# Kernel tuning notes

Measured on AMD Instinct MI355X. Metric: run time of the kernel, lower is better.

Reference implementation:

```python
import jax, jax.numpy as jnp
import numpy as np

INV_DELTA = 15.0  # inv_delta init kwarg


def setup_inputs() -> dict:
    key = jax.random.key(0)
    k1, k2 = jax.random.split(key)
    features = jax.random.normal(k1, (64, 1024, 14, 14), dtype=jnp.float32)
    # torch init: randn(num_words, num_channels).clamp(min=0)
    embedding = jnp.clip(jax.random.normal(k2, (8192, 1024), dtype=jnp.float32), 0.0, None)
    min_distance_mean = jnp.ones((1,), dtype=jnp.float32) * 0.5  # buffer init
    return {"features": features, "embedding": embedding,
            "min_distance_mean": min_distance_mean}


def reference(features, embedding, min_distance_mean):
    # BoWExtractor.forward in eval mode (no dictionary queue update / EMA).
    f = features[:, :, 1:-1, 1:-1]                      # [B,C,12,12] crop border
    emb_sq = jnp.sum(embedding * embedding, axis=1)     # [K]  ||w_k||^2
    cross = jnp.einsum('bchw,kc->bkhw', f, embedding)   # 1x1 conv == GEMM
    # squared L2 distance to every codeword: [B,K,12,12]
    dist = jnp.sum(f * f, axis=1, keepdims=True) - 2.0 * cross \
           + emb_sq[None, :, None, None]
    inv_delta_adaptive = INV_DELTA / min_distance_mean[0]
    codes = jax.nn.softmax(-inv_delta_adaptive * dist, axis=1)  # soft assignment over K
    bow = jnp.max(codes, axis=(2, 3))                   # global max-pool -> [B,K]
    bow = bow / jnp.sum(jnp.abs(bow), axis=1, keepdims=True)  # L1 normalize
    return bow, codes
```

## Files before the change

kernel.cpp:

```cpp
#include <hip/hip_runtime.h>
#include <math.h>

#define BB   64
#define CC   1024
#define HWC  144
#define KK   8192
#define MM   9216
#define NBN  64

typedef __attribute__((ext_vector_type(8))) short          bf16x8;
typedef __attribute__((ext_vector_type(8))) unsigned short u16x8;
typedef __attribute__((ext_vector_type(4))) float          f32x4;

#define FA_BYTES  ((size_t)MM * CC * 2 * 2)
#define FB_BYTES  ((size_t)KK * CC * 2 * 2)
#define OFF_FA    0
#define OFF_FB    (OFF_FA + FA_BYTES)
#define OFF_ESQ   (OFF_FB + FB_BYTES)
#define OFF_PM    (OFF_ESQ + (size_t)KK * 4)
#define OFF_PS    (OFF_PM + (size_t)NBN * MM * 4)
#define OFF_FACT  (OFF_PS + (size_t)NBN * MM * 4)

__device__ inline unsigned short f2bf(float x) {
    union { float f; unsigned u; } v; v.f = x;
    unsigned r = v.u + 0x7fffu + ((v.u >> 16) & 1u);
    return (unsigned short)(r >> 16);
}
__device__ inline float bf2f(unsigned short h) {
    union { unsigned u; float f; } v; v.u = (unsigned)h << 16;
    return v.f;
}

__global__ __launch_bounds__(256)
void prep_A(const float* __restrict__ feat, u16x8* __restrict__ fA) {
    __shared__ float tile[64][145];
    int cb = blockIdx.x;
    int b  = blockIdx.y;
    for (int idx = threadIdx.x; idx < 64 * 144; idx += 256) {
        int r = idx / 144, hw = idx - r * 144;
        int h = hw / 12, w = hw - h * 12;
        tile[r][hw] = feat[(size_t)((b * 1024 + cb * 64 + r) * 196)
                           + (h + 1) * 14 + (w + 1)];
    }
    __syncthreads();
    for (int idx = threadIdx.x; idx < 8 * 144; idx += 256) {
        int g = idx / 144, hw = idx - g * 144;
        int p = b * 144 + hw;
        int bm = p >> 7, row = p & 127;
        int cg = cb * 64 + g * 8;
        int kt = cg >> 5, chunk = (cg >> 3) & 3;
        u16x8 hi, lo;
#pragma unroll
        for (int e = 0; e < 8; ++e) {
            float x = tile[g * 8 + e][hw];
            unsigned short h16 = f2bf(x);
            hi[e] = (short)h16;
            lo[e] = (short)f2bf(x - bf2f(h16));
        }
        size_t base = ((size_t)(bm * 32 + kt) * 2) * 512 + chunk * 128 + row;
        fA[base] = hi;
        fA[base + 512] = lo;
    }
}

__global__ __launch_bounds__(256)
void prep_B(const float* __restrict__ emb, u16x8* __restrict__ fB) {
    __shared__ float tile[128][65];
    int cb = blockIdx.x;
    int bn = blockIdx.y;
#pragma unroll
    for (int i = 0; i < 8; ++i) {
        int idx = threadIdx.x + i * 256;
        int nl = idx >> 4, c4 = idx & 15;
        const float4 v = *reinterpret_cast<const float4*>(
            emb + (size_t)(bn * 128 + nl) * 1024 + cb * 64 + c4 * 4);
        tile[nl][c4 * 4 + 0] = v.x;
        tile[nl][c4 * 4 + 1] = v.y;
        tile[nl][c4 * 4 + 2] = v.z;
        tile[nl][c4 * 4 + 3] = v.w;
    }
    __syncthreads();
#pragma unroll
    for (int i = 0; i < 4; ++i) {
        int idx = threadIdx.x + i * 256;
        int kc = idx >> 7, row = idx & 127;
        int ktl = kc >> 2, chunk = kc & 3;
        int cl = ktl * 32 + chunk * 8;
        u16x8 hi, lo;
#pragma unroll
        for (int e = 0; e < 8; ++e) {
            float x = tile[row][cl + e];
            unsigned short h16 = f2bf(x);
            hi[e] = (short)h16;
            lo[e] = (short)f2bf(x - bf2f(h16));
        }
        int kt = cb * 2 + ktl;
        size_t base = ((size_t)(bn * 32 + kt) * 2) * 512 + chunk * 128 + row;
        fB[base] = hi;
        fB[base + 512] = lo;
    }
}

__global__ void rowsumsq(const float* __restrict__ src, float* __restrict__ dst) {
    int row = blockIdx.x * 4 + (threadIdx.x >> 6);
    int l = threadIdx.x & 63;
    const float4* p = reinterpret_cast<const float4*>(src + (size_t)row * 1024);
    float s = 0.f;
#pragma unroll
    for (int it = 0; it < 4; ++it) {
        float4 v = p[l + it * 64];
        s += v.x * v.x + v.y * v.y + v.z * v.z + v.w * v.w;
    }
#pragma unroll
    for (int off = 32; off; off >>= 1) s += __shfl_down(s, off);
    if (l == 0) dst[row] = s;
}

__global__ __launch_bounds__(256, 2)
void gemm_mfma(const char* __restrict__ fA, const char* __restrict__ fB,
               const float* __restrict__ esq, const float* __restrict__ mdm,
               float* __restrict__ codes, float* __restrict__ pm,
               float* __restrict__ ps) {
    __shared__ __align__(16) char smem[65536];

    int flat = blockIdx.y * 64 + blockIdx.x;
    int swz = (flat & 7) * 576 + (flat >> 3);
    int bm = swz >> 6, bn = swz & 63;

    int tid = threadIdx.x;
    int l = tid & 63, lr = l & 15, lc = l >> 4;
    int wv = tid >> 6, wr = wv >> 1, wc = wv & 1;

    const char* gA = fA + (size_t)(bm * 32) * 16384;
    const char* gB = fB + (size_t)(bn * 32) * 16384;

    f32x4 acc[4][4];
#pragma unroll
    for (int i = 0; i < 4; ++i)
#pragma unroll
        for (int j = 0; j < 4; ++j) acc[i][j] = (f32x4){0.f, 0.f, 0.f, 0.f};

    auto stage = [&](int nb, int kt) {
        char* db = smem + nb * 32768;
        const char* ga = gA + (size_t)kt * 16384;
        const char* gb = gB + (size_t)kt * 16384;
#pragma unroll
        for (int i = 0; i < 4; ++i) {
            int off = (wv * 4 + i) * 1024;
            __builtin_amdgcn_global_load_lds(
                (const __attribute__((address_space(1))) void*)(ga + off + l * 16),
                (__attribute__((address_space(3))) void*)(db + off), 16, 0, 0);
            __builtin_amdgcn_global_load_lds(
                (const __attribute__((address_space(1))) void*)(gb + off + l * 16),
                (__attribute__((address_space(3))) void*)(db + 16384 + off), 16, 0, 0);
        }
    };

    stage(0, 0);
    __syncthreads();
    int cur = 0;
    for (int kt = 0; kt < 32; ++kt) {
        if (kt < 31) stage(cur ^ 1, kt + 1);
        const char* bufc = smem + cur * 32768;
        bf16x8 ahi[4], alo[4], bhi[4], blo[4];
#pragma unroll
        for (int f = 0; f < 4; ++f) {
            int ao = ((lc * 128) + wr * 64 + f * 16 + lr) * 16;
            ahi[f] = *(const bf16x8*)(bufc + ao);
            alo[f] = *(const bf16x8*)(bufc + 8192 + ao);
            int bo = ((lc * 128) + wc * 64 + f * 16 + lr) * 16;
            bhi[f] = *(const bf16x8*)(bufc + 16384 + bo);
            blo[f] = *(const bf16x8*)(bufc + 24576 + bo);
        }
#pragma unroll
        for (int fi = 0; fi < 4; ++fi)
#pragma unroll
            for (int fj = 0; fj < 4; ++fj) {
                acc[fi][fj] = __builtin_amdgcn_mfma_f32_16x16x32_bf16(
                    ahi[fi], bhi[fj], acc[fi][fj], 0, 0, 0);
                acc[fi][fj] = __builtin_amdgcn_mfma_f32_16x16x32_bf16(
                    ahi[fi], blo[fj], acc[fi][fj], 0, 0, 0);
                acc[fi][fj] = __builtin_amdgcn_mfma_f32_16x16x32_bf16(
                    alo[fi], bhi[fj], acc[fi][fj], 0, 0, 0);
            }
        __syncthreads();
        cur ^= 1;
    }

    float invl2 = (15.0f / mdm[0]) * 1.44269504089f;
    float s2 = 2.0f * invl2;
    float e2[4];
#pragma unroll
    for (int fj = 0; fj < 4; ++fj)
        e2[fj] = invl2 * esq[bn * 128 + wc * 64 + fj * 16 + lr];

#pragma unroll
    for (int fi = 0; fi < 4; ++fi)
#pragma unroll
        for (int fj = 0; fj < 4; ++fj)
#pragma unroll
            for (int j = 0; j < 4; ++j)
                acc[fi][fj][j] = s2 * acc[fi][fj][j] - e2[fj];

    float mx[4][4];
#pragma unroll
    for (int fi = 0; fi < 4; ++fi)
#pragma unroll
        for (int j = 0; j < 4; ++j) {
            float m = acc[fi][0][j];
            m = fmaxf(m, acc[fi][1][j]);
            m = fmaxf(m, acc[fi][2][j]);
            m = fmaxf(m, acc[fi][3][j]);
            mx[fi][j] = m;
        }
#pragma unroll
    for (int off = 1; off < 16; off <<= 1)
#pragma unroll
        for (int fi = 0; fi < 4; ++fi)
#pragma unroll
            for (int j = 0; j < 4; ++j)
                mx[fi][j] = fmaxf(mx[fi][j], __shfl_xor(mx[fi][j], off));

    float* sm = (float*)smem;
    if (lr == 0) {
#pragma unroll
        for (int fi = 0; fi < 4; ++fi)
#pragma unroll
            for (int j = 0; j < 4; ++j)
                sm[wc * 128 + wr * 64 + fi * 16 + lc * 4 + j] = mx[fi][j];
    }
    __syncthreads();
    float mp[4][4];
#pragma unroll
    for (int fi = 0; fi < 4; ++fi)
#pragma unroll
        for (int j = 0; j < 4; ++j) {
            int pi = wr * 64 + fi * 16 + lc * 4 + j;
            mp[fi][j] = fmaxf(sm[pi], sm[128 + pi]);
        }

    float ss[4][4];
#pragma unroll
    for (int fi = 0; fi < 4; ++fi)
#pragma unroll
        for (int j = 0; j < 4; ++j) ss[fi][j] = 0.f;
#pragma unroll
    for (int fi = 0; fi < 4; ++fi)
#pragma unroll
        for (int fj = 0; fj < 4; ++fj)
#pragma unroll
            for (int j = 0; j < 4; ++j) {
                float E = exp2f(acc[fi][fj][j] - mp[fi][j]);
                acc[fi][fj][j] = E;
                ss[fi][j] += E;
            }
#pragma unroll
    for (int off = 1; off < 16; off <<= 1)
#pragma unroll
        for (int fi = 0; fi < 4; ++fi)
#pragma unroll
            for (int j = 0; j < 4; ++j)
                ss[fi][j] += __shfl_xor(ss[fi][j], off);
    if (lr == 0) {
#pragma unroll
        for (int fi = 0; fi < 4; ++fi)
#pragma unroll
            for (int j = 0; j < 4; ++j)
                sm[256 + wc * 128 + wr * 64 + fi * 16 + lc * 4 + j] = ss[fi][j];
    }
    __syncthreads();
    if (tid < 128) {
        int p = bm * 128 + tid;
        pm[(size_t)bn * MM + p] = fmaxf(sm[tid], sm[128 + tid]);
        ps[(size_t)bn * MM + p] = sm[256 + tid] + sm[384 + tid];
    }

#pragma unroll
    for (int fi = 0; fi < 4; ++fi) {
        int p0 = bm * 128 + wr * 64 + fi * 16 + lc * 4;
        int b = p0 / 144, hw = p0 - b * 144;
#pragma unroll
        for (int fj = 0; fj < 4; ++fj) {
            int k = bn * 128 + wc * 64 + fj * 16 + lr;
            __builtin_nontemporal_store(
                acc[fi][fj],
                (f32x4*)(codes + ((size_t)(b * 8192 + k)) * 144 + hw));
        }
    }
}

__global__ void comb_factor(const float* __restrict__ pm,
                            const float* __restrict__ ps,
                            float* __restrict__ factor) {
    int p = blockIdx.x * 256 + threadIdx.x;
    float m = -INFINITY;
#pragma unroll 8
    for (int bn = 0; bn < NBN; ++bn) m = fmaxf(m, pm[(size_t)bn * MM + p]);
    float S = 0.f;
#pragma unroll 8
    for (int bn = 0; bn < NBN; ++bn)
        S += ps[(size_t)bn * MM + p] * exp2f(pm[(size_t)bn * MM + p] - m);
    float is = 1.f / S;
#pragma unroll 8
    for (int bn = 0; bn < NBN; ++bn)
        factor[(size_t)bn * MM + p] = exp2f(pm[(size_t)bn * MM + p] - m) * is;
}

__global__ __launch_bounds__(256)
void scale_bow(float* __restrict__ codes, const float* __restrict__ factor,
               float* __restrict__ bow) {
    int wid = threadIdx.x >> 6, l = threadIdx.x & 63;
    int r = blockIdx.x * 4 + wid;
    int b = r >> 13, k = r & 8191;
    f32x4* Cp = (f32x4*)(codes + (size_t)r * 144);
    const f32x4* Fp = (const f32x4*)(factor + (size_t)(k >> 7) * MM + b * 144);
    float m = 0.f;
    if (l < 36) {
        f32x4 e = __builtin_nontemporal_load(Cp + l);
        f32x4 f = Fp[l];
        f32x4 v = e * f;
        __builtin_nontemporal_store(v, Cp + l);
        m = fmaxf(fmaxf(v.x, v.y), fmaxf(v.z, v.w));
    }
#pragma unroll
    for (int off = 32; off; off >>= 1) m = fmaxf(m, __shfl_down(m, off));
    if (l == 0) bow[r] = m;
}

__global__ void bow_norm(float* __restrict__ bow) {
    __shared__ float lds[4];
    __shared__ float stot;
    int b = blockIdx.x;
    float* p = bow + b * 8192;
    float s = 0.f;
    for (int i = threadIdx.x; i < 8192; i += 256) s += fabsf(p[i]);
#pragma unroll
    for (int off = 32; off; off >>= 1) s += __shfl_down(s, off);
    int wid = threadIdx.x >> 6, l = threadIdx.x & 63;
    if (l == 0) lds[wid] = s;
    __syncthreads();
    if (threadIdx.x == 0) stot = 1.f / (lds[0] + lds[1] + lds[2] + lds[3]);
    __syncthreads();
    float inv = stot;
    for (int i = threadIdx.x; i < 8192; i += 256) p[i] *= inv;
}

extern "C" void kernel_launch(void* const* d_in, const int* in_sizes, int n_in,
                              void* d_out, int out_size, void* d_ws, size_t ws_size,
                              hipStream_t stream) {
    const float* feat = (const float*)d_in[0];
    const float* emb  = (const float*)d_in[1];
    const float* mdm  = (const float*)d_in[2];
    float* bow   = (float*)d_out;
    float* codes = (float*)d_out + (size_t)BB * KK;

    char* ws = (char*)d_ws;
    u16x8* fA    = (u16x8*)(ws + OFF_FA);
    u16x8* fB    = (u16x8*)(ws + OFF_FB);
    float* esq   = (float*)(ws + OFF_ESQ);
    float* pm    = (float*)(ws + OFF_PM);
    float* ps    = (float*)(ws + OFF_PS);
    float* fact  = (float*)(ws + OFF_FACT);

    prep_A<<<dim3(16, 64), 256, 0, stream>>>(feat, fA);
    prep_B<<<dim3(16, 64), 256, 0, stream>>>(emb, fB);
    rowsumsq<<<KK / 4, 256, 0, stream>>>(emb, esq);
    gemm_mfma<<<dim3(64, 72), 256, 0, stream>>>((const char*)fA, (const char*)fB,
                                                esq, mdm, codes, pm, ps);
    comb_factor<<<36, 256, 0, stream>>>(pm, ps, fact);
    scale_bow<<<(BB * KK) / 4, 256, 0, stream>>>(codes, fact, bow);
    bow_norm<<<BB, 256, 0, stream>>>(bow);
}
```

Before: 579.0 us.

## Enlarge GEMM tile to 256x256 with 8 waves and deeper LDS prefetch

The split-bf16 GEMM tile grows from 128x128 with 4 waves to 256x256 with 8 waves. The packed A/B layouts and the number of column partial softmax blocks (NBN) are changed to match. The k-loop now keeps two stages in flight using explicit vmcnt waits and raw barriers, and raises wave priority around the MFMA bursts. The goal is more data reuse per LDS byte and better overlap of loads with compute. The cost is 128KB of LDS and one block per CU, which lowers occupancy, plus much higher register pressure from 32 accumulators.

```diff
diff --git a/kernel.cpp b/kernel.cpp
--- a/kernel.cpp
+++ b/kernel.cpp
@@ -6,7 +6,7 @@
 #define HWC  144
 #define KK   8192
 #define MM   9216
-#define NBN  64
+#define NBN  32
 
 typedef __attribute__((ext_vector_type(8))) short          bf16x8;
 typedef __attribute__((ext_vector_type(8))) unsigned short u16x8;
@@ -46,7 +46,7 @@
     for (int idx = threadIdx.x; idx < 8 * 144; idx += 256) {
         int g = idx / 144, hw = idx - g * 144;
         int p = b * 144 + hw;
-        int bm = p >> 7, row = p & 127;
+        int bm = p >> 8, row = p & 255;
         int cg = cb * 64 + g * 8;
         int kt = cg >> 5, chunk = (cg >> 3) & 3;
         u16x8 hi, lo;
@@ -57,9 +57,9 @@
             hi[e] = (short)h16;
             lo[e] = (short)f2bf(x - bf2f(h16));
         }
-        size_t base = ((size_t)(bm * 32 + kt) * 2) * 512 + chunk * 128 + row;
+        size_t base = (size_t)(bm * 32 + kt) * 2048 + chunk * 256 + row;
         fA[base] = hi;
-        fA[base + 512] = lo;
+        fA[base + 1024] = lo;
     }
 }
 
@@ -67,13 +67,13 @@
 void prep_B(const float* __restrict__ emb, u16x8* __restrict__ fB) {
     __shared__ float tile[128][65];
     int cb = blockIdx.x;
-    int bn = blockIdx.y;
+    int nb = blockIdx.y;
 #pragma unroll
     for (int i = 0; i < 8; ++i) {
         int idx = threadIdx.x + i * 256;
         int nl = idx >> 4, c4 = idx & 15;
         const float4 v = *reinterpret_cast<const float4*>(
-            emb + (size_t)(bn * 128 + nl) * 1024 + cb * 64 + c4 * 4);
+            emb + (size_t)(nb * 128 + nl) * 1024 + cb * 64 + c4 * 4);
         tile[nl][c4 * 4 + 0] = v.x;
         tile[nl][c4 * 4 + 1] = v.y;
         tile[nl][c4 * 4 + 2] = v.z;
@@ -83,21 +83,23 @@
 #pragma unroll
     for (int i = 0; i < 4; ++i) {
         int idx = threadIdx.x + i * 256;
-        int kc = idx >> 7, row = idx & 127;
+        int kc = idx >> 7, rl = idx & 127;
         int ktl = kc >> 2, chunk = kc & 3;
         int cl = ktl * 32 + chunk * 8;
+        int n = nb * 128 + rl;
+        int bn = n >> 8, row = n & 255;
         u16x8 hi, lo;
 #pragma unroll
         for (int e = 0; e < 8; ++e) {
-            float x = tile[row][cl + e];
+            float x = tile[rl][cl + e];
             unsigned short h16 = f2bf(x);
             hi[e] = (short)h16;
             lo[e] = (short)f2bf(x - bf2f(h16));
         }
         int kt = cb * 2 + ktl;
-        size_t base = ((size_t)(bn * 32 + kt) * 2) * 512 + chunk * 128 + row;
+        size_t base = (size_t)(bn * 32 + kt) * 2048 + chunk * 256 + row;
         fB[base] = hi;
-        fB[base + 512] = lo;
+        fB[base + 1024] = lo;
     }
 }
 
@@ -116,136 +118,151 @@
     if (l == 0) dst[row] = s;
 }
 
-__global__ __launch_bounds__(256, 2)
+__global__ __launch_bounds__(512, 1)
 void gemm_mfma(const char* __restrict__ fA, const char* __restrict__ fB,
                const float* __restrict__ esq, const float* __restrict__ mdm,
                float* __restrict__ codes, float* __restrict__ pm,
                float* __restrict__ ps) {
-    __shared__ __align__(16) char smem[65536];
-
-    int flat = blockIdx.y * 64 + blockIdx.x;
-    int swz = (flat & 7) * 576 + (flat >> 3);
-    int bm = swz >> 6, bn = swz & 63;
+    __shared__ __align__(16) char smem[131072];
+
+    int flat = blockIdx.x;
+    int swz = (flat & 7) * 144 + (flat >> 3);
+    int bm = swz >> 5, bn = swz & 31;
 
     int tid = threadIdx.x;
     int l = tid & 63, lr = l & 15, lc = l >> 4;
-    int wv = tid >> 6, wr = wv >> 1, wc = wv & 1;
-
-    const char* gA = fA + (size_t)(bm * 32) * 16384;
-    const char* gB = fB + (size_t)(bn * 32) * 16384;
-
-    f32x4 acc[4][4];
-#pragma unroll
-    for (int i = 0; i < 4; ++i)
+    int wv = tid >> 6, wr = wv >> 2, wc = wv & 3;
+
+    const char* gA = fA + (size_t)bm * 1048576;
+    const char* gB = fB + (size_t)bn * 1048576;
+
+    f32x4 acc[8][4];
+#pragma unroll
+    for (int i = 0; i < 8; ++i)
 #pragma unroll
         for (int j = 0; j < 4; ++j) acc[i][j] = (f32x4){0.f, 0.f, 0.f, 0.f};
 
-    auto stage = [&](int nb, int kt) {
-        char* db = smem + nb * 32768;
-        const char* ga = gA + (size_t)kt * 16384;
-        const char* gb = gB + (size_t)kt * 16384;
+    auto stage = [&](int buf, int kt) {
+        char* db = smem + buf * 65536;
+        const char* ga = gA + (size_t)kt * 32768;
+        const char* gb = gB + (size_t)kt * 32768;
 #pragma unroll
         for (int i = 0; i < 4; ++i) {
-            int off = (wv * 4 + i) * 1024;
+            int off = i * 8192 + tid * 16;
             __builtin_amdgcn_global_load_lds(
-                (const __attribute__((address_space(1))) void*)(ga + off + l * 16),
+                (const __attribute__((address_space(1))) void*)(ga + off),
                 (__attribute__((address_space(3))) void*)(db + off), 16, 0, 0);
             __builtin_amdgcn_global_load_lds(
-                (const __attribute__((address_space(1))) void*)(gb + off + l * 16),
-                (__attribute__((address_space(3))) void*)(db + 16384 + off), 16, 0, 0);
+                (const __attribute__((address_space(1))) void*)(gb + off),
+                (__attribute__((address_space(3))) void*)(db + 32768 + off), 16, 0, 0);
         }
     };
 
     stage(0, 0);
-    __syncthreads();
-    int cur = 0;
+    stage(1, 1);
+
     for (int kt = 0; kt < 32; ++kt) {
-        if (kt < 31) stage(cur ^ 1, kt + 1);
-        const char* bufc = smem + cur * 32768;
-        bf16x8 ahi[4], alo[4], bhi[4], blo[4];
-#pragma unroll
-        for (int f = 0; f < 4; ++f) {
-            int ao = ((lc * 128) + wr * 64 + f * 16 + lr) * 16;
-            ahi[f] = *(const bf16x8*)(bufc + ao);
-            alo[f] = *(const bf16x8*)(bufc + 8192 + ao);
-            int bo = ((lc * 128) + wc * 64 + f * 16 + lr) * 16;
-            bhi[f] = *(const bf16x8*)(bufc + 16384 + bo);
-            blo[f] = *(const bf16x8*)(bufc + 24576 + bo);
-        }
-#pragma unroll
-        for (int fi = 0; fi < 4; ++fi)
-#pragma unroll
-            for (int fj = 0; fj < 4; ++fj) {
-                acc[fi][fj] = __builtin_amdgcn_mfma_f32_16x16x32_bf16(
-                    ahi[fi], bhi[fj], acc[fi][fj], 0, 0, 0);
-                acc[fi][fj] = __builtin_amdgcn_mfma_f32_16x16x32_bf16(
-                    ahi[fi], blo[fj], acc[fi][fj], 0, 0, 0);
-                acc[fi][fj] = __builtin_amdgcn_mfma_f32_16x16x32_bf16(
-                    alo[fi], bhi[fj], acc[fi][fj], 0, 0, 0);
+        asm volatile("s_waitcnt vmcnt(8)" ::: "memory");
+        __builtin_amdgcn_s_barrier();
+        __builtin_amdgcn_sched_barrier(0);
+
+        const char* bufc = smem + (kt & 1) * 65536;
+        bf16x8 bh[4], bl[4];
+#pragma unroll
+        for (int fj = 0; fj < 4; ++fj) {
+            int bo = 32768 + lc * 4096 + (wc * 64 + fj * 16 + lr) * 16;
+            bh[fj] = *(const bf16x8*)(bufc + bo);
+            bl[fj] = *(const bf16x8*)(bufc + 16384 + bo);
+        }
+#pragma unroll
+        for (int half = 0; half < 2; ++half) {
+            bf16x8 ah[4], al[4];
+#pragma unroll
+            for (int f = 0; f < 4; ++f) {
+                int ao = lc * 4096 + (wr * 128 + (half * 4 + f) * 16 + lr) * 16;
+                ah[f] = *(const bf16x8*)(bufc + ao);
+                al[f] = *(const bf16x8*)(bufc + 16384 + ao);
             }
-        __syncthreads();
-        cur ^= 1;
-    }
+            __builtin_amdgcn_s_setprio(1);
+#pragma unroll
+            for (int f = 0; f < 4; ++f)
+#pragma unroll
+                for (int fj = 0; fj < 4; ++fj) {
+                    f32x4& A = acc[half * 4 + f][fj];
+                    A = __builtin_amdgcn_mfma_f32_16x16x32_bf16(ah[f], bh[fj], A, 0, 0, 0);
+                    A = __builtin_amdgcn_mfma_f32_16x16x32_bf16(ah[f], bl[fj], A, 0, 0, 0);
+                    A = __builtin_amdgcn_mfma_f32_16x16x32_bf16(al[f], bh[fj], A, 0, 0, 0);
+                }
+            __builtin_amdgcn_s_setprio(0);
+        }
+        __builtin_amdgcn_s_barrier();
+        int kn = (kt + 2 > 31) ? 31 : kt + 2;
+        stage(kt & 1, kn);
+    }
+
+    asm volatile("s_waitcnt vmcnt(0)" ::: "memory");
+    __builtin_amdgcn_s_barrier();
 
     float invl2 = (15.0f / mdm[0]) * 1.44269504089f;
     float s2 = 2.0f * invl2;
     float e2[4];
 #pragma unroll
     for (int fj = 0; fj < 4; ++fj)
-        e2[fj] = invl2 * esq[bn * 128 + wc * 64 + fj * 16 + lr];
-
-#pragma unroll
-    for (int fi = 0; fi < 4; ++fi)
+        e2[fj] = invl2 * esq[bn * 256 + wc * 64 + fj * 16 + lr];
+
+#pragma unroll
+    for (int fi = 0; fi < 8; ++fi)
 #pragma unroll
         for (int fj = 0; fj < 4; ++fj)
 #pragma unroll
             for (int j = 0; j < 4; ++j)
                 acc[fi][fj][j] = s2 * acc[fi][fj][j] - e2[fj];
 
-    float mx[4][4];
-#pragma unroll
-    for (int fi = 0; fi < 4; ++fi)
+    float mx[8][4];
+#pragma unroll
+    for (int fi = 0; fi < 8; ++fi)
 #pragma unroll
         for (int j = 0; j < 4; ++j) {
-            float m = acc[fi][0][j];
-            m = fmaxf(m, acc[fi][1][j]);
-            m = fmaxf(m, acc[fi][2][j]);
-            m = fmaxf(m, acc[fi][3][j]);
+            float m = fmaxf(fmaxf(acc[fi][0][j], acc[fi][1][j]),
+                            fmaxf(acc[fi][2][j], acc[fi][3][j]));
             mx[fi][j] = m;
         }
 #pragma unroll
     for (int off = 1; off < 16; off <<= 1)
 #pragma unroll
-        for (int fi = 0; fi < 4; ++fi)
+        for (int fi = 0; fi < 8; ++fi)
 #pragma unroll
             for (int j = 0; j < 4; ++j)
                 mx[fi][j] = fmaxf(mx[fi][j], __shfl_xor(mx[fi][j], off));
 
-    float* sm = (float*)smem;
+    float* maxb = (float*)smem;
+    float* sumb = (float*)smem + 1024;
     if (lr == 0) {
 #pragma unroll
-        for (int fi = 0; fi < 4; ++fi)
-#pragma unroll
-            for (int j = 0; j < 4; ++j)
-                sm[wc * 128 + wr * 64 + fi * 16 + lc * 4 + j] = mx[fi][j];
-    }
-    __syncthreads();
-    float mp[4][4];
-#pragma unroll
-    for (int fi = 0; fi < 4; ++fi)
+        for (int fi = 0; fi < 8; ++fi)
+#pragma unroll
+            for (int j = 0; j < 4; ++j)
+                maxb[wc * 256 + wr * 128 + fi * 16 + lc * 4 + j] = mx[fi][j];
+    }
+    __syncthreads();
+
+    float mp[8][4];
+#pragma unroll
+    for (int fi = 0; fi < 8; ++fi)
 #pragma unroll
         for (int j = 0; j < 4; ++j) {
-            int pi = wr * 64 + fi * 16 + lc * 4 + j;
-            mp[fi][j] = fmaxf(sm[pi], sm[128 + pi]);
-        }
-
-    float ss[4][4];
-#pragma unroll
-    for (int fi = 0; fi < 4; ++fi)
+            int row = wr * 128 + fi * 16 + lc * 4 + j;
+            mp[fi][j] = fmaxf(fmaxf(maxb[row], maxb[256 + row]),
+                              fmaxf(maxb[512 + row], maxb[768 + row]));
+        }
+
+    float ss[8][4];
+#pragma unroll
+    for (int fi = 0; fi < 8; ++fi)
 #pragma unroll
         for (int j = 0; j < 4; ++j) ss[fi][j] = 0.f;
 #pragma unroll
-    for (int fi = 0; fi < 4; ++fi)
+    for (int fi = 0; fi < 8; ++fi)
 #pragma unroll
         for (int fj = 0; fj < 4; ++fj)
 #pragma unroll
@@ -257,31 +274,33 @@
 #pragma unroll
     for (int off = 1; off < 16; off <<= 1)
 #pragma unroll
-        for (int fi = 0; fi < 4; ++fi)
+        for (int fi = 0; fi < 8; ++fi)
 #pragma unroll
             for (int j = 0; j < 4; ++j)
                 ss[fi][j] += __shfl_xor(ss[fi][j], off);
     if (lr == 0) {
 #pragma unroll
-        for (int fi = 0; fi < 4; ++fi)
-#pragma unroll
-            for (int j = 0; j < 4; ++j)
-                sm[256 + wc * 128 + wr * 64 + fi * 16 + lc * 4 + j] = ss[fi][j];
-    }
-    __syncthreads();
-    if (tid < 128) {
-        int p = bm * 128 + tid;
-        pm[(size_t)bn * MM + p] = fmaxf(sm[tid], sm[128 + tid]);
-        ps[(size_t)bn * MM + p] = sm[256 + tid] + sm[384 + tid];
-    }
-
-#pragma unroll
-    for (int fi = 0; fi < 4; ++fi) {
-        int p0 = bm * 128 + wr * 64 + fi * 16 + lc * 4;
+        for (int fi = 0; fi < 8; ++fi)
+#pragma unroll
+            for (int j = 0; j < 4; ++j)
+                sumb[wc * 256 + wr * 128 + fi * 16 + lc * 4 + j] = ss[fi][j];
+    }
+    __syncthreads();
+    if (tid < 256) {
+        int p = bm * 256 + tid;
+        pm[(size_t)bn * MM + p] = fmaxf(fmaxf(maxb[tid], maxb[256 + tid]),
+                                        fmaxf(maxb[512 + tid], maxb[768 + tid]));
+        ps[(size_t)bn * MM + p] = sumb[tid] + sumb[256 + tid]
+                                + sumb[512 + tid] + sumb[768 + tid];
+    }
+
+#pragma unroll
+    for (int fi = 0; fi < 8; ++fi) {
+        int p0 = bm * 256 + wr * 128 + fi * 16 + lc * 4;
         int b = p0 / 144, hw = p0 - b * 144;
 #pragma unroll
         for (int fj = 0; fj < 4; ++fj) {
-            int k = bn * 128 + wc * 64 + fj * 16 + lr;
+            int k = bn * 256 + wc * 64 + fj * 16 + lr;
             __builtin_nontemporal_store(
                 acc[fi][fj],
                 (f32x4*)(codes + ((size_t)(b * 8192 + k)) * 144 + hw));
@@ -313,7 +332,7 @@
     int r = blockIdx.x * 4 + wid;
     int b = r >> 13, k = r & 8191;
     f32x4* Cp = (f32x4*)(codes + (size_t)r * 144);
-    const f32x4* Fp = (const f32x4*)(factor + (size_t)(k >> 7) * MM + b * 144);
+    const f32x4* Fp = (const f32x4*)(factor + (size_t)(k >> 8) * MM + b * 144);
     float m = 0.f;
     if (l < 36) {
         f32x4 e = __builtin_nontemporal_load(Cp + l);
@@ -365,8 +384,8 @@
     prep_A<<<dim3(16, 64), 256, 0, stream>>>(feat, fA);
     prep_B<<<dim3(16, 64), 256, 0, stream>>>(emb, fB);
     rowsumsq<<<KK / 4, 256, 0, stream>>>(emb, esq);
-    gemm_mfma<<<dim3(64, 72), 256, 0, stream>>>((const char*)fA, (const char*)fB,
-                                                esq, mdm, codes, pm, ps);
+    gemm_mfma<<<1152, 512, 0, stream>>>((const char*)fA, (const char*)fB,
+                                        esq, mdm, codes, pm, ps);
     comb_factor<<<36, 256, 0, stream>>>(pm, ps, fact);
     scale_bow<<<(BB * KK) / 4, 256, 0, stream>>>(codes, fact, bow);
     bow_norm<<<BB, 256, 0, stream>>>(bow);
```

New measurement: 607.4 us. 4.9% more time.
